# Kernel tuning notes

Hardware: AMD Instinct MI355X
Metric: run time of the kernel (lower is better)

The kernel has to match this reference:

```python
import jax, jax.numpy as jnp
import numpy as np

B, S, D = 4, 2048, 2048
H, K = 16, 128          # num_heads, intermediate_dim
FINAL = H * K           # 2048
VDIM = 2048             # vector_dim
EPS_LN = 1e-6
EPS_NORM = 1e-30


def setup_inputs() -> dict:
    key = jax.random.key(0)
    ks = jax.random.split(key, 8)
    x = jax.random.normal(ks[0], (B, S, D), dtype=jnp.float32)
    vector = jax.random.normal(ks[1], (B, VDIM), dtype=jnp.float32)
    W_att = jax.random.normal(ks[2], (D, H), dtype=jnp.float32) / np.sqrt(D)
    temperature = jnp.ones((1, 1, H), dtype=jnp.float32)
    W_values = jax.random.normal(ks[3], (D, H, K), dtype=jnp.float32) / np.sqrt(D)
    W_op = jax.random.normal(ks[4], (FINAL, VDIM), dtype=jnp.float32) / np.sqrt(FINAL)
    ff1 = jax.random.normal(ks[5], (VDIM + D, D), dtype=jnp.float32) / np.sqrt(VDIM + D)
    ff1_b = jnp.zeros((1, 1, D), dtype=jnp.float32)
    ff2 = jax.random.normal(ks[6], (D, D), dtype=jnp.float32) / np.sqrt(D)
    ff2_b = jnp.zeros((1, 1, D), dtype=jnp.float32)
    gamma = jnp.ones((D,), dtype=jnp.float32)
    beta = jnp.zeros((D,), dtype=jnp.float32)
    return {"x": x, "vector": vector, "W_att": W_att, "temperature": temperature,
            "W_values": W_values, "W_op": W_op, "ff1": ff1, "ff1_b": ff1_b,
            "ff2": ff2, "ff2_b": ff2_b, "gamma": gamma, "beta": beta}


def reference(x, vector, W_att, temperature, W_values, W_op, ff1, ff1_b, ff2, ff2_b, gamma, beta):
    b, s, d = x.shape
    # attention gate per (query) position -- [B,S,H]
    logits = jnp.matmul(x, W_att)
    logits = logits - jnp.max(logits, axis=-2, keepdims=True)
    w = jnp.exp(logits * temperature)
    # exact collapse of repeat+tril+normalize: A[b,i,j,h] = w[b,i,h]*tril[i,j]
    # denom[b,i,h] = w[b,i,h]*(i+1) + 1e-30  ->  out = coef * causal cumsum of v
    counts = jnp.arange(1, s + 1, dtype=x.dtype)[None, :, None]  # [1,S,1]
    coef = w / (w * counts + EPS_NORM)                            # [B,S,H]
    v = jnp.einsum('bsi,ihk->bshk', x, W_values)                  # [B,S,H,K]
    cum_v = jnp.cumsum(v, axis=1)                                 # prefix-sum over keys
    pooled = (coef[..., None] * cum_v).reshape(b, s, -1)          # [B,S,H*K]
    op = jnp.matmul(pooled, W_op) + vector[:, None, :]            # [B,S,VDIM]
    concat = jnp.concatenate([x, op], axis=-1)                    # [B,S,VDIM+D]
    h = jax.nn.relu(jnp.matmul(concat, ff1) + ff1_b)
    h = jax.nn.relu(jnp.matmul(h, ff2) + ff2_b)
    res = h + x
    mean = jnp.mean(res, axis=-1, keepdims=True)
    cen = res - mean
    var = jnp.mean(cen * cen, axis=-1, keepdims=True)
    return cen / jnp.sqrt(var + EPS_LN) * gamma + beta
```

## Files before the change

kernel.cpp:

```cpp
#include <hip/hip_runtime.h>
#include <stdint.h>

#define B_DIM 4
#define S_DIM 2048
#define D_DIM 2048
#define H_DIM 16
#define M_ROWS (B_DIM * S_DIM)
#define CONCAT_LD 4096
#define NCHUNK 32
#define CHLEN (S_DIM / NCHUNK)

#define BM 128
#define BN 128
#define BK 64

typedef __attribute__((ext_vector_type(8))) __bf16 bf16x8;
typedef __attribute__((ext_vector_type(4))) float f32x4;

__device__ inline unsigned short f2bf(float f) {
  union { float f; unsigned u; } x; x.f = f;
  unsigned r = x.u + 0x7fffu + ((x.u >> 16) & 1u);
  return (unsigned short)(r >> 16);
}
__device__ inline float bf2f(unsigned short s) {
  union { unsigned u; float f; } x; x.u = ((unsigned)s) << 16;
  return x.f;
}

__global__ __launch_bounds__(256) void xconv_logits_kernel(
    const float* __restrict__ x, const float* __restrict__ Watt,
    unsigned short* __restrict__ concat, float* __restrict__ logits) {
  int row = blockIdx.x, t = threadIdx.x;
  const float* xr = x + (size_t)row * D_DIM;
  unsigned short* cr = concat + (size_t)row * CONCAT_LD;
  float p[H_DIM];
#pragma unroll
  for (int h = 0; h < H_DIM; ++h) p[h] = 0.f;
#pragma unroll
  for (int i = 0; i < 8; ++i) {
    int k = t + i * 256;
    float xv = xr[k];
    cr[k] = f2bf(xv);
    const float* wr = Watt + (size_t)k * H_DIM;
#pragma unroll
    for (int h = 0; h < H_DIM; ++h) p[h] += xv * wr[h];
  }
  __shared__ float red[4][H_DIM];
  int l = t & 63, w = t >> 6;
#pragma unroll
  for (int h = 0; h < H_DIM; ++h) {
    float v = p[h];
    for (int off = 32; off; off >>= 1) v += __shfl_down(v, off);
    if (l == 0) red[w][h] = v;
  }
  __syncthreads();
  if (t < H_DIM)
    logits[(size_t)row * H_DIM + t] = red[0][t] + red[1][t] + red[2][t] + red[3][t];
}

__global__ __launch_bounds__(256) void transpose_conv_kernel(
    const float* __restrict__ src, unsigned short* __restrict__ dst,
    int R, int C, int ldd) {
  __shared__ float tile[32][33];
  int c0 = blockIdx.x * 32, r0 = blockIdx.y * 32;
  int tx = threadIdx.x & 31, ty = threadIdx.x >> 5;
#pragma unroll
  for (int i = 0; i < 32; i += 8)
    tile[ty + i][tx] = src[(size_t)(r0 + ty + i) * C + c0 + tx];
  __syncthreads();
#pragma unroll
  for (int i = 0; i < 32; i += 8)
    dst[(size_t)(c0 + ty + i) * ldd + r0 + tx] = f2bf(tile[tx][ty + i]);
}

__global__ __launch_bounds__(256) void convert_kernel(
    const float* __restrict__ src, unsigned short* __restrict__ dst) {
  int idx = (blockIdx.x * 256 + threadIdx.x) * 4;
  const float4 v = *(const float4*)(src + idx);
  ushort4 o;
  o.x = f2bf(v.x); o.y = f2bf(v.y); o.z = f2bf(v.z); o.w = f2bf(v.w);
  *(ushort4*)(dst + idx) = o;
}

__global__ __launch_bounds__(256) void coef_kernel(
    const float* __restrict__ logits, const float* __restrict__ temp, float* __restrict__ coef) {
  int b = blockIdx.x >> 4, h = blockIdx.x & 15;
  int t = threadIdx.x;
  const float* lg = logits + (size_t)b * S_DIM * H_DIM + h;
  float mx = -1e30f;
  for (int s = t; s < S_DIM; s += 256) mx = fmaxf(mx, lg[(size_t)s * H_DIM]);
  for (int off = 32; off; off >>= 1) mx = fmaxf(mx, __shfl_down(mx, off));
  __shared__ float red[4];
  if ((t & 63) == 0) red[t >> 6] = mx;
  __syncthreads();
  mx = fmaxf(fmaxf(red[0], red[1]), fmaxf(red[2], red[3]));
  float T = temp[h];
  float* cf = coef + (size_t)b * S_DIM * H_DIM + h;
  for (int s = t; s < S_DIM; s += 256) {
    float w = expf((lg[(size_t)s * H_DIM] - mx) * T);
    cf[(size_t)s * H_DIM] = w / (w * (float)(s + 1) + 1e-30f);
  }
}

__global__ __launch_bounds__(256) void bias2_partial_kernel(
    const float* __restrict__ vector, const float* __restrict__ ff1,
    float* __restrict__ part) {
  int n = blockIdx.x * 256 + threadIdx.x;
  int seg = blockIdx.y, b = blockIdx.z;
  const float* vr = vector + (size_t)b * 2048 + seg * 128;
  const float* fr = ff1 + (size_t)(2048 + seg * 128) * 2048 + n;
  float acc = 0.f;
#pragma unroll 8
  for (int j = 0; j < 128; ++j) acc += vr[j] * fr[(size_t)j * 2048];
  part[((size_t)seg * 4 + b) * 2048 + n] = acc;
}

__global__ __launch_bounds__(256) void bias2_reduce_kernel(
    const float* __restrict__ part, const float* __restrict__ ff1_b,
    float* __restrict__ bias2) {
  int n = blockIdx.x * 256 + threadIdx.x;
  int b = blockIdx.y;
  float acc = ff1_b[n];
#pragma unroll
  for (int s = 0; s < 16; ++s) acc += part[((size_t)s * 4 + b) * 2048 + n];
  bias2[(size_t)b * 2048 + n] = acc;
}

template <int MODE>
__global__ __launch_bounds__(256) void gemm_bt_kernel(
    const unsigned short* __restrict__ A, int lda,
    const unsigned short* __restrict__ Bt, int ldb, int K,
    void* __restrict__ outp, int ldo,
    const float* __restrict__ bias, const float* __restrict__ resid) {
  __shared__ unsigned short As[BM * BK];
  __shared__ unsigned short Bs[BN * BK];
  const int t = threadIdx.x;
  const int w = t >> 6, l = t & 63;
  const int wm = w & 1, wn = w >> 1;
  const int q = l >> 4, ln = l & 15;

  const int L = blockIdx.y * 16 + blockIdx.x;
  const int xcd = L & 7;
  const int W = L >> 3;
  const int bx = W & 15;
  const int by = (W >> 4) * 8 + xcd;
  const int m0 = by * BM, n0 = bx * BN;

  f32x4 acc[4][4];
#pragma unroll
  for (int i = 0; i < 4; ++i)
#pragma unroll
    for (int j = 0; j < 4; ++j) acc[i][j] = {0.f, 0.f, 0.f, 0.f};

  for (int k0 = 0; k0 < K; k0 += BK) {
    __syncthreads();
#pragma unroll
    for (int r = 0; r < 4; ++r) {
      int s = r * 256 + t;
      int row = s >> 3;
      int ch = (s & 7) ^ (row & 7);
      const unsigned short* ga = A + (size_t)(m0 + row) * lda + k0 + ch * 8;
      __builtin_amdgcn_global_load_lds(
          (const __attribute__((address_space(1))) void*)ga,
          (__attribute__((address_space(3))) void*)(As + (r * 256 + w * 64) * 8), 16, 0, 0);
      const unsigned short* gb = Bt + (size_t)(n0 + row) * ldb + k0 + ch * 8;
      __builtin_amdgcn_global_load_lds(
          (const __attribute__((address_space(1))) void*)gb,
          (__attribute__((address_space(3))) void*)(Bs + (r * 256 + w * 64) * 8), 16, 0, 0);
    }
    __syncthreads();
#pragma unroll
    for (int h = 0; h < 2; ++h) {
      bf16x8 af[4], bfr[4];
#pragma unroll
      for (int mt = 0; mt < 4; ++mt) {
        int ar = wm * 64 + mt * 16 + ln;
        af[mt] = *(const bf16x8*)&As[ar * BK + (((h * 4 + q) ^ (ar & 7)) * 8)];
      }
#pragma unroll
      for (int nt = 0; nt < 4; ++nt) {
        int br = wn * 64 + nt * 16 + ln;
        bfr[nt] = *(const bf16x8*)&Bs[br * BK + (((h * 4 + q) ^ (br & 7)) * 8)];
      }
#pragma unroll
      for (int mt = 0; mt < 4; ++mt)
#pragma unroll
        for (int nt = 0; nt < 4; ++nt)
          acc[mt][nt] = __builtin_amdgcn_mfma_f32_16x16x32_bf16(af[mt], bfr[nt], acc[mt][nt], 0, 0, 0);
    }
  }

#pragma unroll
  for (int mt = 0; mt < 4; ++mt) {
#pragma unroll
    for (int i = 0; i < 4; ++i) {
      int row = m0 + wm * 64 + mt * 16 + q * 4 + i;
#pragma unroll
      for (int nt = 0; nt < 4; ++nt) {
        int col = n0 + wn * 64 + nt * 16 + ln;
        float vv = acc[mt][nt][i];
        if (MODE == 2) { vv += bias[(size_t)(row >> 11) * 2048 + col]; vv = fmaxf(vv, 0.f); }
        if (MODE == 4) {
          vv += bias[col]; vv = fmaxf(vv, 0.f);
          vv += resid[(size_t)row * 2048 + col];
          ((float*)outp)[(size_t)row * ldo + col] = vv;
        } else {
          ((unsigned short*)outp)[(size_t)row * ldo + col] = f2bf(vv);
        }
      }
    }
  }
}

__global__ __launch_bounds__(256) void scan_partial_kernel(
    const unsigned short* __restrict__ v, float* __restrict__ csum) {
  int c = blockIdx.x * 256 + threadIdx.x;
  int chunk = blockIdx.y, b = blockIdx.z;
  const unsigned short* p = v + ((size_t)(b * S_DIM + chunk * CHLEN)) * D_DIM + c;
  float s = 0.f;
#pragma unroll 4
  for (int i = 0; i < CHLEN; ++i) s += bf2f(p[(size_t)i * D_DIM]);
  csum[((size_t)b * NCHUNK + chunk) * D_DIM + c] = s;
}

__global__ __launch_bounds__(256) void scan_offsets_kernel(float* __restrict__ csum) {
  int c = blockIdx.x * 256 + threadIdx.x;
  int b = blockIdx.y;
  float run = 0.f;
  float* p = csum + (size_t)b * NCHUNK * D_DIM + c;
  for (int ch = 0; ch < NCHUNK; ++ch) {
    float tv = p[(size_t)ch * D_DIM];
    p[(size_t)ch * D_DIM] = run;
    run += tv;
  }
}

__global__ __launch_bounds__(256) void scan_apply_kernel(
    const unsigned short* __restrict__ v, const float* __restrict__ csum,
    const float* __restrict__ coef, unsigned short* __restrict__ pooled_out) {
  int c = blockIdx.x * 256 + threadIdx.x;
  int chunk = blockIdx.y, b = blockIdx.z;
  int h = c >> 7;
  int row0 = b * S_DIM + chunk * CHLEN;
  float run = csum[((size_t)b * NCHUNK + chunk) * D_DIM + c];
  const unsigned short* vp = v + (size_t)row0 * D_DIM + c;
  unsigned short* po = pooled_out + (size_t)row0 * CONCAT_LD + c;
  const float* cf = coef + (size_t)row0 * H_DIM + h;
#pragma unroll 4
  for (int i = 0; i < CHLEN; ++i) {
    run += bf2f(vp[(size_t)i * D_DIM]);
    po[(size_t)i * CONCAT_LD] = f2bf(cf[(size_t)i * H_DIM] * run);
  }
}

__global__ __launch_bounds__(256) void ln_kernel(
    float* __restrict__ out, const float* __restrict__ gamma, const float* __restrict__ beta) {
  int row = blockIdx.x, t = threadIdx.x;
  float* pr = out + (size_t)row * D_DIM;
  float vals[8];
  float s = 0.f;
#pragma unroll
  for (int i = 0; i < 8; ++i) { vals[i] = pr[t + i * 256]; s += vals[i]; }
  __shared__ float red[4];
  for (int off = 32; off; off >>= 1) s += __shfl_down(s, off);
  if ((t & 63) == 0) red[t >> 6] = s;
  __syncthreads();
  float mean = (red[0] + red[1] + red[2] + red[3]) * (1.f / D_DIM);
  __syncthreads();
  float c2 = 0.f;
#pragma unroll
  for (int i = 0; i < 8; ++i) { float c = vals[i] - mean; c2 += c * c; }
  for (int off = 32; off; off >>= 1) c2 += __shfl_down(c2, off);
  if ((t & 63) == 0) red[t >> 6] = c2;
  __syncthreads();
  float var = (red[0] + red[1] + red[2] + red[3]) * (1.f / D_DIM);
  float rstd = rsqrtf(var + 1e-6f);
#pragma unroll
  for (int i = 0; i < 8; ++i) {
    int col = t + i * 256;
    pr[col] = (vals[i] - mean) * rstd * gamma[col] + beta[col];
  }
}

extern "C" void kernel_launch(void* const* d_in, const int* in_sizes, int n_in,
                              void* d_out, int out_size, void* d_ws, size_t ws_size,
                              hipStream_t stream) {
  const float* x      = (const float*)d_in[0];
  const float* vector = (const float*)d_in[1];
  const float* W_att  = (const float*)d_in[2];
  const float* temp   = (const float*)d_in[3];
  const float* W_val  = (const float*)d_in[4];
  const float* W_op   = (const float*)d_in[5];
  const float* ff1    = (const float*)d_in[6];
  const float* ff1_b  = (const float*)d_in[7];
  const float* ff2    = (const float*)d_in[8];
  const float* ff2_b  = (const float*)d_in[9];
  const float* gamma  = (const float*)d_in[10];
  const float* beta   = (const float*)d_in[11];
  float* out = (float*)d_out;

  char* ws = (char*)d_ws;
  auto alloc = [&](size_t bytes) {
    char* p = ws; ws += (bytes + 255) & ~(size_t)255; return p;
  };
  unsigned short* concat = (unsigned short*)alloc((size_t)M_ROWS * CONCAT_LD * 2);
  unsigned short* wv_t   = (unsigned short*)alloc((size_t)2048 * 2048 * 2);
  unsigned short* btff1  = (unsigned short*)alloc((size_t)2048 * 4096 * 2);
  unsigned short* f1bT   = (unsigned short*)alloc((size_t)2048 * 2048 * 2);
  unsigned short* wop_bf = (unsigned short*)alloc((size_t)2048 * 2048 * 2);
  unsigned short* ff2_t  = (unsigned short*)alloc((size_t)2048 * 2048 * 2);
  unsigned short* vbuf   = (unsigned short*)alloc((size_t)M_ROWS * 2048 * 2);
  unsigned short* h1     = (unsigned short*)alloc((size_t)M_ROWS * 2048 * 2);
  float* logits = (float*)alloc((size_t)M_ROWS * H_DIM * 4);
  float* coef   = (float*)alloc((size_t)M_ROWS * H_DIM * 4);
  float* csum   = (float*)alloc((size_t)B_DIM * NCHUNK * D_DIM * 4);
  float* part   = (float*)alloc((size_t)16 * 4 * 2048 * 4);
  float* bias2  = (float*)alloc((size_t)4 * 2048 * 4);

  xconv_logits_kernel<<<M_ROWS, 256, 0, stream>>>(x, W_att, concat, logits);
  transpose_conv_kernel<<<dim3(64, 64), 256, 0, stream>>>(W_val, wv_t, 2048, 2048, 2048);
  transpose_conv_kernel<<<dim3(64, 64), 256, 0, stream>>>(ff1, btff1, 2048, 2048, 4096);
  transpose_conv_kernel<<<dim3(64, 64), 256, 0, stream>>>(ff1 + (size_t)2048 * 2048, f1bT, 2048, 2048, 2048);
  convert_kernel<<<2048 * 2048 / 1024, 256, 0, stream>>>(W_op, wop_bf);
  transpose_conv_kernel<<<dim3(64, 64), 256, 0, stream>>>(ff2, ff2_t, 2048, 2048, 2048);
  coef_kernel<<<B_DIM * H_DIM, 256, 0, stream>>>(logits, temp, coef);
  gemm_bt_kernel<1><<<dim3(16, 16), 256, 0, stream>>>(
      f1bT, 2048, wop_bf, 2048, 2048, btff1 + 2048, 4096, nullptr, nullptr);
  bias2_partial_kernel<<<dim3(8, 16, 4), 256, 0, stream>>>(vector, ff1, part);
  bias2_reduce_kernel<<<dim3(8, 4), 256, 0, stream>>>(part, ff1_b, bias2);
  gemm_bt_kernel<1><<<dim3(16, 64), 256, 0, stream>>>(
      concat, CONCAT_LD, wv_t, 2048, 2048, vbuf, 2048, nullptr, nullptr);
  scan_partial_kernel<<<dim3(8, NCHUNK, B_DIM), 256, 0, stream>>>(vbuf, csum);
  scan_offsets_kernel<<<dim3(8, B_DIM), 256, 0, stream>>>(csum);
  scan_apply_kernel<<<dim3(8, NCHUNK, B_DIM), 256, 0, stream>>>(vbuf, csum, coef, concat + 2048);
  gemm_bt_kernel<2><<<dim3(16, 64), 256, 0, stream>>>(
      concat, CONCAT_LD, btff1, 4096, 4096, h1, 2048, bias2, nullptr);
  gemm_bt_kernel<4><<<dim3(16, 64), 256, 0, stream>>>(
      h1, 2048, ff2_t, 2048, 2048, out, 2048, ff2_b, x);
  ln_kernel<<<M_ROWS, 256, 0, stream>>>(out, gamma, beta);
}
```

Before: 720.9 us.

## Add 256x256-tile GEMM with direct-to-LDS loads and pipelined half-K stages

Adds a new GEMM kernel that uses 256x256 output tiles and 512 threads, staging A and B straight into LDS with global_load_lds. The K loop is split into half-tiles, with explicit vmcnt waits and barriers so loads overlap the MFMA work, and the block order is swizzled. The three large GEMMs (values, ff1, ff2) now use it in place of the 128x128 kernel, to get more operand reuse and hide memory latency. Costs are heavier LDS and register pressure and fragile hand-placed synchronisation.

```diff
diff --git a/kernel.cpp b/kernel.cpp
--- a/kernel.cpp
+++ b/kernel.cpp
@@ -195,6 +195,139 @@
 #pragma unroll
     for (int i = 0; i < 4; ++i) {
       int row = m0 + wm * 64 + mt * 16 + q * 4 + i;
+#pragma unroll
+      for (int nt = 0; nt < 4; ++nt) {
+        int col = n0 + wn * 64 + nt * 16 + ln;
+        float vv = acc[mt][nt][i];
+        if (MODE == 2) { vv += bias[(size_t)(row >> 11) * 2048 + col]; vv = fmaxf(vv, 0.f); }
+        if (MODE == 4) {
+          vv += bias[col]; vv = fmaxf(vv, 0.f);
+          vv += resid[(size_t)row * 2048 + col];
+          ((float*)outp)[(size_t)row * ldo + col] = vv;
+        } else {
+          ((unsigned short*)outp)[(size_t)row * ldo + col] = f2bf(vv);
+        }
+      }
+    }
+  }
+}
+
+#define GLD16(g, s)                                                        \
+  __builtin_amdgcn_global_load_lds(                                        \
+      (const __attribute__((address_space(1))) void*)(g),                  \
+      (__attribute__((address_space(3))) void*)(s), 16, 0, 0)
+#define BARX() asm volatile("s_barrier" ::: "memory")
+#define VMW8() asm volatile("s_waitcnt vmcnt(8)" ::: "memory")
+#define VMW0() asm volatile("s_waitcnt vmcnt(0)" ::: "memory")
+
+template <int MODE>
+__global__ __launch_bounds__(512, 2) void gemm256_kernel(
+    const unsigned short* __restrict__ A, int lda,
+    const unsigned short* __restrict__ Bt, int ldb, int K,
+    void* __restrict__ outp, int ldo,
+    const float* __restrict__ bias, const float* __restrict__ resid) {
+  __shared__ unsigned short As[2][2][256 * 32];
+  __shared__ unsigned short Bs[2][2][256 * 32];
+  const int t = threadIdx.x;
+  const int wv = t >> 6, l = t & 63;
+  const int wm = wv >> 2, wn = wv & 3;
+  const int q = l >> 4, ln = l & 15;
+
+  const int L = blockIdx.y * 8 + blockIdx.x;
+  const int lin = (L & 7) * 32 + (L >> 3);
+  const int m0 = (lin >> 3) * 256, n0 = (lin & 7) * 256;
+
+  const int srow = t >> 2;
+  const int scol = (((t & 3) * 16) ^ (((srow >> 1) & 3) << 4)) >> 1;
+  const unsigned short* Abase = A + (size_t)(m0 + srow) * lda + scol;
+  const unsigned short* Bbase = Bt + (size_t)(n0 + srow) * ldb + scol;
+  const size_t astep = (size_t)128 * lda, bstep = (size_t)128 * ldb;
+  const int axor = ((ln >> 1) & 3) << 3;
+
+  f32x4 acc[8][4];
+#pragma unroll
+  for (int i = 0; i < 8; ++i)
+#pragma unroll
+    for (int j = 0; j < 4; ++j) acc[i][j] = {0.f, 0.f, 0.f, 0.f};
+
+  auto stageA = [&](int kt, int kh, int buf) {
+    const unsigned short* g = Abase + (size_t)kt * 64 + kh * 32;
+    GLD16(g, &As[buf][kh][wv * 512]);
+    GLD16(g + astep, &As[buf][kh][4096 + wv * 512]);
+  };
+  auto stageB = [&](int kt, int kh, int buf) {
+    const unsigned short* g = Bbase + (size_t)kt * 64 + kh * 32;
+    GLD16(g, &Bs[buf][kh][wv * 512]);
+    GLD16(g + bstep, &Bs[buf][kh][4096 + wv * 512]);
+  };
+
+  bf16x8 a[8], b[2];
+  auto loadA = [&](int buf, int h) {
+#pragma unroll
+    for (int mt = 0; mt < 8; ++mt) {
+      int ar = wm * 128 + mt * 16 + ln;
+      a[mt] = *(const bf16x8*)&As[buf][h][ar * 32 + ((q * 8) ^ axor)];
+    }
+  };
+  auto loadB2 = [&](int buf, int h, int np) {
+#pragma unroll
+    for (int i = 0; i < 2; ++i) {
+      int br = wn * 64 + (np * 2 + i) * 16 + ln;
+      b[i] = *(const bf16x8*)&Bs[buf][h][br * 32 + ((q * 8) ^ axor)];
+    }
+  };
+  auto mm = [&](int np) {
+    __builtin_amdgcn_s_setprio(1);
+#pragma unroll
+    for (int mt = 0; mt < 8; ++mt)
+#pragma unroll
+      for (int i = 0; i < 2; ++i)
+        acc[mt][np * 2 + i] =
+            __builtin_amdgcn_mfma_f32_16x16x32_bf16(a[mt], b[i], acc[mt][np * 2 + i], 0, 0, 0);
+    __builtin_amdgcn_s_setprio(0);
+  };
+
+  const int NT = K >> 6;
+  stageA(0, 0, 0); stageB(0, 0, 0);
+  stageA(0, 1, 0); stageB(0, 1, 0);
+  stageA(1, 0, 1); stageB(1, 0, 1);
+  VMW8();
+  BARX();
+
+  for (int tt = 0; tt < NT; ++tt) {
+    const int c = tt & 1;
+    const int t1 = (tt + 1 == NT) ? 0 : tt + 1;
+    const int t2 = (tt + 2 >= NT) ? tt + 2 - NT : tt + 2;
+    loadA(c, 0); loadB2(c, 0, 0);
+    stageA(t1, 1, c ^ 1);
+    BARX();
+    mm(0);
+    BARX();
+    loadB2(c, 0, 1);
+    stageB(t1, 1, c ^ 1);
+    BARX();
+    mm(1);
+    VMW8();
+    BARX();
+    loadA(c, 1); loadB2(c, 1, 0);
+    stageA(t2, 0, c);
+    BARX();
+    mm(0);
+    BARX();
+    loadB2(c, 1, 1);
+    stageB(t2, 0, c);
+    BARX();
+    mm(1);
+    VMW8();
+    BARX();
+  }
+  VMW0();
+
+#pragma unroll
+  for (int mt = 0; mt < 8; ++mt) {
+#pragma unroll
+    for (int i = 0; i < 4; ++i) {
+      int row = m0 + wm * 128 + mt * 16 + q * 4 + i;
 #pragma unroll
       for (int nt = 0; nt < 4; ++nt) {
         int col = n0 + wn * 64 + nt * 16 + ln;
@@ -328,14 +461,14 @@
       f1bT, 2048, wop_bf, 2048, 2048, btff1 + 2048, 4096, nullptr, nullptr);
   bias2_partial_kernel<<<dim3(8, 16, 4), 256, 0, stream>>>(vector, ff1, part);
   bias2_reduce_kernel<<<dim3(8, 4), 256, 0, stream>>>(part, ff1_b, bias2);
-  gemm_bt_kernel<1><<<dim3(16, 64), 256, 0, stream>>>(
+  gemm256_kernel<1><<<dim3(8, 32), 512, 0, stream>>>(
       concat, CONCAT_LD, wv_t, 2048, 2048, vbuf, 2048, nullptr, nullptr);
   scan_partial_kernel<<<dim3(8, NCHUNK, B_DIM), 256, 0, stream>>>(vbuf, csum);
   scan_offsets_kernel<<<dim3(8, B_DIM), 256, 0, stream>>>(csum);
   scan_apply_kernel<<<dim3(8, NCHUNK, B_DIM), 256, 0, stream>>>(vbuf, csum, coef, concat + 2048);
-  gemm_bt_kernel<2><<<dim3(16, 64), 256, 0, stream>>>(
+  gemm256_kernel<2><<<dim3(8, 32), 512, 0, stream>>>(
       concat, CONCAT_LD, btff1, 4096, 4096, h1, 2048, bias2, nullptr);
-  gemm_bt_kernel<4><<<dim3(16, 64), 256, 0, stream>>>(
+  gemm256_kernel<4><<<dim3(8, 32), 512, 0, stream>>>(
       h1, 2048, ff2_t, 2048, 2048, out, 2048, ff2_b, x);
   ln_kernel<<<M_ROWS, 256, 0, stream>>>(out, gamma, beta);
 }
```

New measurement: 664.7 us. -7.8%, faster.
